# Optimization experiments

Measured on AMD Instinct MI355X. Metric: run time of the kernel, lower is better.

Reference implementation:

```python
import jax, jax.numpy as jnp
import numpy as np

DIM = 1024
EPS_LN = 1e-5
EPS_MEM = 1e-6

def _layernorm(x, g, b):
    mu = jnp.mean(x, axis=-1, keepdims=True)
    var = jnp.mean((x - mu) ** 2, axis=-1, keepdims=True)
    return (x - mu) * jax.lax.rsqrt(var + EPS_LN) * g + b

def setup_inputs() -> dict:
    key = jax.random.key(0)
    ks = jax.random.split(key, 8)
    B, S, D = 4, 4096, DIM
    s1 = 1.0 / np.sqrt(D)
    s2 = 1.0 / np.sqrt(4 * D)
    return {
        "x": jax.random.normal(ks[0], (B, S, D), dtype=jnp.float32),
        "ln1_g": jnp.ones((D,), jnp.float32),
        "ln1_b": jnp.zeros((D,), jnp.float32),
        "ln2_g": jnp.ones((D,), jnp.float32),
        "ln2_b": jnp.zeros((D,), jnp.float32),
        "gate_w": jax.random.uniform(ks[1], (D, D), jnp.float32, -s1, s1),
        "gate_b": jax.random.uniform(ks[2], (D,), jnp.float32, -s1, s1),
        "value_w": jax.random.uniform(ks[3], (D, D), jnp.float32, -s1, s1),
        "value_b": jax.random.uniform(ks[4], (D,), jnp.float32, -s1, s1),
        "ffn_w1": jax.random.uniform(ks[5], (D, 4 * D), jnp.float32, -s1, s1),
        "ffn_b1": jnp.zeros((4 * D,), jnp.float32),
        "ffn_w2": jax.random.uniform(ks[6], (4 * D, D), jnp.float32, -s2, s2),
        "ffn_b2": jnp.zeros((D,), jnp.float32),
    }

def reference(x, ln1_g, ln1_b, ln2_g, ln2_b, gate_w, gate_b, value_w, value_b, ffn_w1, ffn_b1, ffn_w2, ffn_b2):
    h = _layernorm(x, ln1_g, ln1_b)
    g = jax.nn.sigmoid(h @ gate_w + gate_b)
    v = h @ value_w + value_b
    cumsum_v = jnp.cumsum(g * v, axis=1)
    cumsum_g = jnp.cumsum(g, axis=1) + EPS_MEM
    x = x + cumsum_v / cumsum_g
    h2 = _layernorm(x, ln2_g, ln2_b)
    ffn = jax.nn.gelu(h2 @ ffn_w1 + ffn_b1, approximate=False) @ ffn_w2 + ffn_b2
    return x + ffn
```

## Files before the change

kernel.cpp:

```cpp
#include <hip/hip_runtime.h>
#include <cstdint>
#include <cstddef>

#define D_MODEL 1024
#define SEQ     4096
#define BATCH   4
#define M_ROWS  (BATCH*SEQ)
#define NCHUNK  64
#define LCHUNK  (SEQ/NCHUNK)

typedef __bf16 bf16_t;
typedef __bf16 bf16x8 __attribute__((ext_vector_type(8)));
typedef __bf16 bf16x4 __attribute__((ext_vector_type(4)));
typedef float  f32x4  __attribute__((ext_vector_type(4)));

__device__ __forceinline__ void load_lds_128(const bf16_t* g, bf16_t* l) {
    __builtin_amdgcn_global_load_lds(
        (const __attribute__((address_space(1))) unsigned int*)g,
        (__attribute__((address_space(3))) unsigned int*)l,
        16, 0, 0);
}

__device__ __forceinline__ float2 bf16pair_to_f2(unsigned int u) {
    union { unsigned int i; float f; } a, b;
    a.i = u << 16;
    b.i = u & 0xffff0000u;
    float2 r; r.x = a.f; r.y = b.f; return r;
}

__device__ __forceinline__ float gelu_f(float x) {
    float t = x * x;
    float u = x * (1.5957691216f + 0.07135481627f * t);
    return x / (1.0f + __expf(-u));
}

__global__ __launch_bounds__(256)
void transpose_all(const float* __restrict__ gate_w, const float* __restrict__ value_w,
                   const float* __restrict__ ffn_w1, const float* __restrict__ ffn_w2,
                   bf16_t* __restrict__ wgv_t, bf16_t* __restrict__ w1_t,
                   bf16_t* __restrict__ w2_t) {
    int id = blockIdx.x;
    const float* in; bf16_t* outp; int R, C, bx, by;
    if (id < 1024)      { in = gate_w;  outp = wgv_t;               R = 1024; C = 1024; bx = id & 31;  by = id >> 5; }
    else if (id < 2048) { id -= 1024; in = value_w; outp = wgv_t + 1024*1024; R = 1024; C = 1024; bx = id & 31;  by = id >> 5; }
    else if (id < 6144) { id -= 2048; in = ffn_w1;  outp = w1_t;    R = 1024; C = 4096; bx = id & 127; by = id >> 7; }
    else                { id -= 6144; in = ffn_w2;  outp = w2_t;    R = 4096; C = 1024; bx = id & 31;  by = id >> 5; }
    __shared__ float t[32][33];
    int tx = threadIdx.x & 31, ty = threadIdx.x >> 5;
    int c0 = bx * 32, r0 = by * 32;
    #pragma unroll
    for (int j = 0; j < 32; j += 8)
        t[ty + j][tx] = in[(size_t)(r0 + ty + j) * C + c0 + tx];
    __syncthreads();
    #pragma unroll
    for (int j = 0; j < 32; j += 8)
        outp[(size_t)(c0 + ty + j) * R + r0 + tx] = (bf16_t)t[tx][ty + j];
}

__global__ __launch_bounds__(256)
void ln_kernel(const float* __restrict__ x, const float* __restrict__ gamma,
               const float* __restrict__ beta, bf16_t* __restrict__ h) {
    int row = blockIdx.x;
    int tid = threadIdx.x;
    const float4* xr = (const float4*)(x + (size_t)row * D_MODEL);
    float4 v = xr[tid];
    float s  = v.x + v.y + v.z + v.w;
    float ss = v.x*v.x + v.y*v.y + v.z*v.z + v.w*v.w;
    #pragma unroll
    for (int off = 32; off; off >>= 1) {
        s  += __shfl_down(s, off);
        ss += __shfl_down(ss, off);
    }
    __shared__ float red[8];
    int wave = tid >> 6, lane = tid & 63;
    if (lane == 0) { red[wave] = s; red[4 + wave] = ss; }
    __syncthreads();
    if (tid == 0) {
        float S  = red[0] + red[1] + red[2] + red[3];
        float SS = red[4] + red[5] + red[6] + red[7];
        float mean = S * (1.0f / D_MODEL);
        float var  = SS * (1.0f / D_MODEL) - mean * mean;
        red[0] = mean;
        red[1] = rsqrtf(var + 1e-5f);
    }
    __syncthreads();
    float mean = red[0], rstd = red[1];
    float4 gv = ((const float4*)gamma)[tid];
    float4 bv = ((const float4*)beta)[tid];
    bf16x4 o;
    o[0] = (bf16_t)((v.x - mean) * rstd * gv.x + bv.x);
    o[1] = (bf16_t)((v.y - mean) * rstd * gv.y + bv.y);
    o[2] = (bf16_t)((v.z - mean) * rstd * gv.z + bv.z);
    o[3] = (bf16_t)((v.w - mean) * rstd * gv.w + bv.w);
    ((bf16x4*)h)[(size_t)row * (D_MODEL / 4) + tid] = o;
}

#define PHASE_MID() do { __builtin_amdgcn_s_barrier(); \
    asm volatile("s_waitcnt lgkmcnt(0)" ::: "memory"); \
    __builtin_amdgcn_s_setprio(1); } while (0)
#define PHASE_END() do { __builtin_amdgcn_s_setprio(0); \
    __builtin_amdgcn_s_barrier(); } while (0)
#define PHASE_END_VM() do { __builtin_amdgcn_s_setprio(0); \
    asm volatile("s_waitcnt vmcnt(4)" ::: "memory"); \
    __builtin_amdgcn_s_barrier(); } while (0)

#define LDA4(BUF, MB) do { _Pragma("unroll") for (int m_ = 0; m_ < 4; ++m_) { \
    af[m_][0] = *(const bf16x8*)((BUF) + aoff0 + ((MB)*4 + m_) * 1024); \
    af[m_][1] = *(const bf16x8*)((BUF) + aoff1 + ((MB)*4 + m_) * 1024); } } while (0)
#define LDB2(BUF, NLO) do { _Pragma("unroll") for (int n_ = 0; n_ < 2; ++n_) { \
    bfr[(NLO)+n_][0] = *(const bf16x8*)((BUF) + boff0 + ((NLO)+n_) * 1024); \
    bfr[(NLO)+n_][1] = *(const bf16x8*)((BUF) + boff1 + ((NLO)+n_) * 1024); } } while (0)
#define MFMA_HALF(MB, NLO) do { _Pragma("unroll") for (int m_ = 0; m_ < 4; ++m_) { \
    _Pragma("unroll") for (int n_ = 0; n_ < 2; ++n_) { \
        acc[(MB)*4 + m_][(NLO) + n_] = __builtin_amdgcn_mfma_f32_16x16x32_bf16( \
            bfr[(NLO)+n_][0], af[m_][0], acc[(MB)*4 + m_][(NLO) + n_], 0, 0, 0); \
        acc[(MB)*4 + m_][(NLO) + n_] = __builtin_amdgcn_mfma_f32_16x16x32_bf16( \
            bfr[(NLO)+n_][1], af[m_][1], acc[(MB)*4 + m_][(NLO) + n_], 0, 0, 0); } } } while (0)

template <int MODE, int TN, int TPB, int LKT>
__global__ __launch_bounds__(512, 2)
void gemm256(const bf16_t* __restrict__ A, const bf16_t* __restrict__ Bt,
             const float* __restrict__ bias, const float* __restrict__ bias2,
             const float* __restrict__ xres,
             void* __restrict__ out, void* __restrict__ out2,
             int M, int N, int K) {
    __shared__ __align__(16) bf16_t lds[2][2][256 * 64];

    const int KT = 1 << LKT;
    const int S  = TPB * KT;
    const int NI = S >> 1;

    const int tid  = threadIdx.x;
    const int lane = tid & 63;
    const int wave = tid >> 6;
    const int wm   = wave >> 2;
    const int wn   = wave & 3;

    const int L    = blockIdx.x;
    const int i    = L >> 3;
    const int ngrp = i & 3;
    const int mb   = (L & 7) + 8 * (i >> 2);
    const int m0   = mb * 256;
    const int n00  = ngrp * TPB * 256;

    f32x4 acc[8][4];
    #pragma unroll
    for (int ii = 0; ii < 8; ii++)
        #pragma unroll
        for (int j = 0; j < 4; j++) acc[ii][j] = (f32x4){0.f, 0.f, 0.f, 0.f};

    const int rr = tid >> 3;
    const int sc = ((tid & 7) ^ (rr & 7)) * 8;
    const bf16_t* pa0 = A  + ((size_t)(m0  + rr)) * K + sc;
    const bf16_t* pb0 = Bt + ((size_t)(n00 + rr)) * K + sc;
    const size_t rstep   = (size_t)64 * K;
    const size_t hstep   = rstep * 2;
    const size_t nstride = (size_t)256 * K;

    #define PA(s) (pa0 + (((s) & (KT - 1)) << 6))
    #define PB(s) (pb0 + (size_t)((s) >> LKT) * nstride + (((s) & (KT - 1)) << 6))

    const int l16 = lane & 15, quad = lane >> 4, swz = l16 & 7;
    const int aoff0 = (wm*128 + l16)*64 + ((quad    ) ^ swz)*8;
    const int aoff1 = (wm*128 + l16)*64 + ((quad + 4) ^ swz)*8;
    const int boff0 = (wn*64  + l16)*64 + ((quad    ) ^ swz)*8;
    const int boff1 = (wn*64  + l16)*64 + ((quad + 4) ^ swz)*8;

    bf16_t* LA0 = &lds[0][0][0]; bf16_t* LB0 = &lds[0][1][0];
    bf16_t* LA1 = &lds[1][0][0]; bf16_t* LB1 = &lds[1][1][0];

    auto STAGE = [&](const bf16_t* gsrc, bf16_t* dst) {
        load_lds_128(gsrc,         dst + tid * 8);
        load_lds_128(gsrc + rstep, dst + 4096 + tid * 8);
    };

    STAGE(PB(0),         LB0);
    STAGE(PB(0) + hstep, LB0 + 8192);
    STAGE(PA(0),         LA0);
    STAGE(PA(0) + hstep, LA0 + 8192);
    STAGE(PB(1),         LB1);
    STAGE(PB(1) + hstep, LB1 + 8192);
    asm volatile("s_waitcnt vmcnt(4)" ::: "memory");
    __builtin_amdgcn_s_barrier();

    #pragma unroll 1
    for (int it = 0; it < NI; ++it) {
        const int s1 = 2*it + 1;
        const int s2 = (2*it + 2 < S) ? 2*it + 2 : S - 1;
        const int s3 = (2*it + 3 < S) ? 2*it + 3 : S - 1;
        const bf16_t* a1 = PA(s1);
        const bf16_t* a2 = PA(s2);
        const bf16_t* b2 = PB(s2);
        const bf16_t* b3 = PB(s3);

        bf16x8 af[4][2], bfr[4][2];

        LDA4(LA0, 0); LDB2(LB0, 0);
        STAGE(a1, LA1);
        PHASE_MID(); MFMA_HALF(0, 0); PHASE_END();
        LDB2(LB0, 2);
        STAGE(a1 + hstep, LA1 + 8192);
        PHASE_MID(); MFMA_HALF(0, 2); PHASE_END();
        LDA4(LA0, 1);
        STAGE(b2, LB0);
        PHASE_MID(); MFMA_HALF(1, 0); PHASE_END();
        STAGE(b2 + hstep, LB0 + 8192);
        PHASE_MID(); MFMA_HALF(1, 2); PHASE_END_VM();
        LDA4(LA1, 0); LDB2(LB1, 0);
        STAGE(a2, LA0);
        PHASE_MID(); MFMA_HALF(0, 0); PHASE_END();
        LDB2(LB1, 2);
        STAGE(a2 + hstep, LA0 + 8192);
        PHASE_MID(); MFMA_HALF(0, 2); PHASE_END();
        LDA4(LA1, 1);
        STAGE(b3, LB1);
        PHASE_MID(); MFMA_HALF(1, 0); PHASE_END();
        STAGE(b3 + hstep, LB1 + 8192);
        PHASE_MID(); MFMA_HALF(1, 2); PHASE_END_VM();

        if (((it + 1) & ((KT >> 1) - 1)) == 0) {
            const int tdone = (2*it + 1) >> LKT;
            const int nn0 = n00 + tdone * 256;
            #pragma unroll
            for (int mt = 0; mt < 8; ++mt) {
                int row = m0 + wm * 128 + mt * 16 + l16;
                #pragma unroll
                for (int nt = 0; nt < 4; ++nt) {
                    int col = nn0 + wn * 64 + nt * 16 + quad * 4;
                    f32x4 a = acc[mt][nt];
                    if (MODE == 4) {
                        bool isV = (nn0 >= 1024);
                        int c1 = col & 1023;
                        float4 bv = *(const float4*)((isV ? bias2 : bias) + c1);
                        float4 val;
                        val.x = a[0] + bv.x; val.y = a[1] + bv.y;
                        val.z = a[2] + bv.z; val.w = a[3] + bv.w;
                        if (!isV) {
                            val.x = 1.0f / (1.0f + __expf(-val.x));
                            val.y = 1.0f / (1.0f + __expf(-val.y));
                            val.z = 1.0f / (1.0f + __expf(-val.z));
                            val.w = 1.0f / (1.0f + __expf(-val.w));
                        }
                        bf16x4 p;
                        p[0] = (bf16_t)val.x; p[1] = (bf16_t)val.y;
                        p[2] = (bf16_t)val.z; p[3] = (bf16_t)val.w;
                        bf16_t* o = (bf16_t*)(isV ? out2 : out);
                        *(bf16x4*)(o + (size_t)row * 1024 + c1) = p;
                    } else if (MODE == 2) {
                        float4 bv = *(const float4*)(bias + col);
                        bf16x4 p;
                        p[0] = (bf16_t)gelu_f(a[0] + bv.x);
                        p[1] = (bf16_t)gelu_f(a[1] + bv.y);
                        p[2] = (bf16_t)gelu_f(a[2] + bv.z);
                        p[3] = (bf16_t)gelu_f(a[3] + bv.w);
                        *(bf16x4*)((bf16_t*)out + (size_t)row * N + col) = p;
                    } else {
                        float4 bv = *(const float4*)(bias + col);
                        float4 xr = *(const float4*)(xres + (size_t)row * N + col);
                        float4 val;
                        val.x = xr.x + a[0] + bv.x; val.y = xr.y + a[1] + bv.y;
                        val.z = xr.z + a[2] + bv.z; val.w = xr.w + a[3] + bv.w;
                        *(float4*)((float*)out + (size_t)row * N + col) = val;
                    }
                    acc[mt][nt] = (f32x4){0.f, 0.f, 0.f, 0.f};
                }
            }
        }
    }

    asm volatile("s_waitcnt vmcnt(0)" ::: "memory");
    #undef PA
    #undef PB
}

__global__ __launch_bounds__(256)
void scan_partial(const bf16_t* __restrict__ g, const bf16_t* __restrict__ v,
                  float* __restrict__ sg, float* __restrict__ sgv) {
    int dt = blockIdx.x & 1;
    int c  = (blockIdx.x >> 1) & (NCHUNK - 1);
    int b  = blockIdx.x >> 7;
    int d  = dt * 512 + threadIdx.x * 2;
    float s0 = 0.f, s1 = 0.f, t0 = 0.f, t1 = 0.f;
    for (int i = 0; i < LCHUNK; i++) {
        int s = c * LCHUNK + i;
        size_t idx = ((size_t)(b * SEQ + s)) * D_MODEL + d;
        float2 gf = bf16pair_to_f2(*(const unsigned int*)(g + idx));
        float2 vf = bf16pair_to_f2(*(const unsigned int*)(v + idx));
        s0 += gf.x; s1 += gf.y;
        t0 += gf.x * vf.x; t1 += gf.y * vf.y;
    }
    size_t o = ((size_t)(b * NCHUNK + c)) * D_MODEL + d;
    sg[o] = s0;  sg[o + 1] = s1;
    sgv[o] = t0; sgv[o + 1] = t1;
}

__global__ __launch_bounds__(256)
void scan_apply(const bf16_t* __restrict__ g, const bf16_t* __restrict__ v,
                const float* __restrict__ x, const float* __restrict__ sg,
                const float* __restrict__ sgv, float* __restrict__ out) {
    int dt = blockIdx.x & 1;
    int c  = (blockIdx.x >> 1) & (NCHUNK - 1);
    int b  = blockIdx.x >> 7;
    int d  = dt * 512 + threadIdx.x * 2;
    float rg0 = 0.f, rg1 = 0.f, rv0 = 0.f, rv1 = 0.f;
    for (int p = 0; p < c; p++) {
        size_t o = ((size_t)(b * NCHUNK + p)) * D_MODEL + d;
        float2 a  = *(const float2*)(sg + o);
        float2 bb = *(const float2*)(sgv + o);
        rg0 += a.x;  rg1 += a.y;
        rv0 += bb.x; rv1 += bb.y;
    }
    for (int i = 0; i < LCHUNK; i++) {
        int s = c * LCHUNK + i;
        size_t idx = ((size_t)(b * SEQ + s)) * D_MODEL + d;
        float2 gf = bf16pair_to_f2(*(const unsigned int*)(g + idx));
        float2 vf = bf16pair_to_f2(*(const unsigned int*)(v + idx));
        rv0 += gf.x * vf.x; rg0 += gf.x;
        rv1 += gf.y * vf.y; rg1 += gf.y;
        float2 xv = *(const float2*)(x + idx);
        float2 ov;
        ov.x = xv.x + rv0 / (rg0 + 1e-6f);
        ov.y = xv.y + rv1 / (rg1 + 1e-6f);
        *(float2*)(out + idx) = ov;
    }
}

extern "C" void kernel_launch(void* const* d_in, const int* in_sizes, int n_in,
                              void* d_out, int out_size, void* d_ws, size_t ws_size,
                              hipStream_t stream) {
    (void)in_sizes; (void)n_in; (void)out_size; (void)ws_size;
    const float* x       = (const float*)d_in[0];
    const float* ln1_g   = (const float*)d_in[1];
    const float* ln1_b   = (const float*)d_in[2];
    const float* ln2_g   = (const float*)d_in[3];
    const float* ln2_b   = (const float*)d_in[4];
    const float* gate_w  = (const float*)d_in[5];
    const float* gate_b  = (const float*)d_in[6];
    const float* value_w = (const float*)d_in[7];
    const float* value_b = (const float*)d_in[8];
    const float* ffn_w1  = (const float*)d_in[9];
    const float* ffn_b1  = (const float*)d_in[10];
    const float* ffn_w2  = (const float*)d_in[11];
    const float* ffn_b2  = (const float*)d_in[12];
    float* out = (float*)d_out;

    char* ws = (char*)d_ws;
    const size_t MB = 1024 * 1024;
    bf16_t* wgv_t = (bf16_t*)(ws + 0 * MB);
    bf16_t* w1_t  = (bf16_t*)(ws + 4 * MB);
    bf16_t* w2_t  = (bf16_t*)(ws + 12 * MB);
    bf16_t* h     = (bf16_t*)(ws + 20 * MB);
    bf16_t* g     = (bf16_t*)(ws + 52 * MB);
    bf16_t* v     = (bf16_t*)(ws + 84 * MB);
    float*  sg    = (float*)(ws + 116 * MB);
    float*  sgv   = (float*)(ws + 117 * MB);
    bf16_t* act   = (bf16_t*)(ws + 118 * MB);

    transpose_all<<<10240, 256, 0, stream>>>(gate_w, value_w, ffn_w1, ffn_w2,
                                             wgv_t, w1_t, w2_t);

    ln_kernel<<<M_ROWS, 256, 0, stream>>>(x, ln1_g, ln1_b, h);

    gemm256<4, 8, 2, 4><<<256, 512, 0, stream>>>(
        h, wgv_t, gate_b, value_b, nullptr, g, v, M_ROWS, 2048, 1024);

    scan_partial<<<BATCH * NCHUNK * 2, 256, 0, stream>>>(g, v, sg, sgv);
    scan_apply<<<BATCH * NCHUNK * 2, 256, 0, stream>>>(g, v, x, sg, sgv, out);

    ln_kernel<<<M_ROWS, 256, 0, stream>>>(out, ln2_g, ln2_b, h);

    gemm256<2, 16, 4, 4><<<256, 512, 0, stream>>>(
        h, w1_t, ffn_b1, nullptr, nullptr, act, nullptr, M_ROWS, 4096, 1024);

    gemm256<3, 4, 1, 6><<<256, 512, 0, stream>>>(
        act, w2_t, ffn_b2, nullptr, out, out, nullptr, M_ROWS, 1024, 4096);
}
```

Measured before the change: 596.5 us.

## Merge GEMM pipeline phases to halve barriers per k-step

Restructures the GEMM main loop from eight fine-grained phases into four coarser phases. Each phase issues both global-to-LDS stages and loads all B fragments at once, then runs two MFMA halves back to back. It also drops the explicit lgkmcnt(0) waits in favour of compiler fences, which halves the barrier count and lets LDS reads overlap more. In exchange, register pressure rises from holding four B fragments, and the changed placement of the vmcnt waits risks LDS read/write hazards if the ordering assumptions are wrong.

```diff
diff --git a/kernel.cpp b/kernel.cpp
--- a/kernel.cpp
+++ b/kernel.cpp
@@ -95,21 +95,19 @@
     ((bf16x4*)h)[(size_t)row * (D_MODEL / 4) + tid] = o;
 }
 
-#define PHASE_MID() do { __builtin_amdgcn_s_barrier(); \
-    asm volatile("s_waitcnt lgkmcnt(0)" ::: "memory"); \
+#define FENCE() asm volatile("" ::: "memory")
+#define SP_MID() do { FENCE(); __builtin_amdgcn_s_barrier(); FENCE(); \
     __builtin_amdgcn_s_setprio(1); } while (0)
-#define PHASE_END() do { __builtin_amdgcn_s_setprio(0); \
-    __builtin_amdgcn_s_barrier(); } while (0)
-#define PHASE_END_VM() do { __builtin_amdgcn_s_setprio(0); \
-    asm volatile("s_waitcnt vmcnt(4)" ::: "memory"); \
-    __builtin_amdgcn_s_barrier(); } while (0)
+#define SP_END() do { __builtin_amdgcn_s_setprio(0); FENCE(); \
+    __builtin_amdgcn_s_barrier(); FENCE(); } while (0)
+#define VMW4() asm volatile("s_waitcnt vmcnt(4)" ::: "memory")
 
 #define LDA4(BUF, MB) do { _Pragma("unroll") for (int m_ = 0; m_ < 4; ++m_) { \
     af[m_][0] = *(const bf16x8*)((BUF) + aoff0 + ((MB)*4 + m_) * 1024); \
     af[m_][1] = *(const bf16x8*)((BUF) + aoff1 + ((MB)*4 + m_) * 1024); } } while (0)
-#define LDB2(BUF, NLO) do { _Pragma("unroll") for (int n_ = 0; n_ < 2; ++n_) { \
-    bfr[(NLO)+n_][0] = *(const bf16x8*)((BUF) + boff0 + ((NLO)+n_) * 1024); \
-    bfr[(NLO)+n_][1] = *(const bf16x8*)((BUF) + boff1 + ((NLO)+n_) * 1024); } } while (0)
+#define LDB4(BUF) do { _Pragma("unroll") for (int n_ = 0; n_ < 4; ++n_) { \
+    bfr[n_][0] = *(const bf16x8*)((BUF) + boff0 + n_ * 1024); \
+    bfr[n_][1] = *(const bf16x8*)((BUF) + boff1 + n_ * 1024); } } while (0)
 #define MFMA_HALF(MB, NLO) do { _Pragma("unroll") for (int m_ = 0; m_ < 4; ++m_) { \
     _Pragma("unroll") for (int n_ = 0; n_ < 2; ++n_) { \
         acc[(MB)*4 + m_][(NLO) + n_] = __builtin_amdgcn_mfma_f32_16x16x32_bf16( \
@@ -180,8 +178,11 @@
     STAGE(PA(0) + hstep, LA0 + 8192);
     STAGE(PB(1),         LB1);
     STAGE(PB(1) + hstep, LB1 + 8192);
-    asm volatile("s_waitcnt vmcnt(4)" ::: "memory");
+    VMW4();
     __builtin_amdgcn_s_barrier();
+    FENCE();
+
+    bf16x8 af[4][2], bfr[4][2];
 
     #pragma unroll 1
     for (int it = 0; it < NI; ++it) {
@@ -193,30 +194,24 @@
         const bf16_t* b2 = PB(s2);
         const bf16_t* b3 = PB(s3);
 
-        bf16x8 af[4][2], bfr[4][2];
-
-        LDA4(LA0, 0); LDB2(LB0, 0);
-        STAGE(a1, LA1);
-        PHASE_MID(); MFMA_HALF(0, 0); PHASE_END();
-        LDB2(LB0, 2);
+        STAGE(a1,         LA1);
         STAGE(a1 + hstep, LA1 + 8192);
-        PHASE_MID(); MFMA_HALF(0, 2); PHASE_END();
+        LDA4(LA0, 0); LDB4(LB0);
+        SP_MID(); MFMA_HALF(0, 0); MFMA_HALF(0, 2); SP_END();
+        STAGE(b2,         LB0);
+        STAGE(b2 + hstep, LB0 + 8192);
         LDA4(LA0, 1);
-        STAGE(b2, LB0);
-        PHASE_MID(); MFMA_HALF(1, 0); PHASE_END();
-        STAGE(b2 + hstep, LB0 + 8192);
-        PHASE_MID(); MFMA_HALF(1, 2); PHASE_END_VM();
-        LDA4(LA1, 0); LDB2(LB1, 0);
-        STAGE(a2, LA0);
-        PHASE_MID(); MFMA_HALF(0, 0); PHASE_END();
-        LDB2(LB1, 2);
+        VMW4();
+        SP_MID(); MFMA_HALF(1, 0); MFMA_HALF(1, 2); SP_END();
+        STAGE(a2,         LA0);
         STAGE(a2 + hstep, LA0 + 8192);
-        PHASE_MID(); MFMA_HALF(0, 2); PHASE_END();
+        LDA4(LA1, 0); LDB4(LB1);
+        SP_MID(); MFMA_HALF(0, 0); MFMA_HALF(0, 2); SP_END();
+        STAGE(b3,         LB1);
+        STAGE(b3 + hstep, LB1 + 8192);
         LDA4(LA1, 1);
-        STAGE(b3, LB1);
-        PHASE_MID(); MFMA_HALF(1, 0); PHASE_END();
-        STAGE(b3 + hstep, LB1 + 8192);
-        PHASE_MID(); MFMA_HALF(1, 2); PHASE_END_VM();
+        VMW4();
+        SP_MID(); MFMA_HALF(1, 0); MFMA_HALF(1, 2); SP_END();
 
         if (((it + 1) & ((KT >> 1) - 1)) == 0) {
             const int tdone = (2*it + 1) >> LKT;
```

After: 599.0 us. No clear change (+0.4%).
